# Optimization experiments

Hardware: AMD Instinct MI355X
Metric: run time of the kernel (lower is better)

Reference implementation:

```python
import jax, jax.numpy as jnp
from jax import lax
import numpy as np

B, H, W, C = 8, 32, 32, 256
SOFTMAX_SCALE = 10.0
DN = ('NHWC', 'HWIO', 'NHWC')


def _patches(t):
    # t: [b,h,w,c] -> [b,h,w,3,3,c], SAME zero padding, stride 1 (tf.image.extract_patches)
    b, h, w, c = t.shape
    tp = jnp.pad(t, ((0, 0), (1, 1), (1, 1), (0, 0)))
    cols = [tp[:, i:i + h, j:j + w, :] for i in range(3) for j in range(3)]
    return jnp.stack(cols, axis=3).reshape(b, h, w, 3, 3, c)


def _diag_fuse(z):
    # conv2d of [L,L] map with eye(3) kernel, SAME padding:
    # out[i,j] = z[i-1,j-1] + z[i,j] + z[i+1,j+1] (zero padded)
    dr = jnp.pad(z, ((1, 0), (1, 0)))[:-1, :-1]
    ul = jnp.pad(z, ((0, 1), (0, 1)))[1:, 1:]
    return z + dr + ul


def _conv(x, w):
    return lax.conv_general_dilated(x, w, (1, 1), 'SAME', dimension_numbers=DN)


def _attend(xi, wi, mmean):
    # xi: [h,w,c]; wi: [3,3,c,L] patch kernels; mmean: [L] mean of mask patches
    h, w, c = xi.shape
    L = h * w
    norm = jnp.maximum(jnp.sqrt(jnp.sum(wi * wi, axis=(0, 1, 2))), 1e-4)
    yi = _conv(xi[None], wi / norm)[0]  # [h,w,L] cosine-sim scores
    # fuse: diagonal propagation along both spatial orderings
    z = yi.reshape(L, L)
    z = _diag_fuse(z).reshape(h, w, h, w).transpose(1, 0, 3, 2).reshape(L, L)
    z = _diag_fuse(z).reshape(w, h, w, h).transpose(1, 0, 3, 2)  # [h,w,h,w]
    yi = z.reshape(h, w, L)
    mm = (mmean == 1.0).astype(yi.dtype)  # valid-patch mask per location
    yi = jax.nn.softmax(yi * mm * SOFTMAX_SCALE, axis=-1) * mm
    # conv2d_transpose(yi, wi, stride 1, SAME) == conv with hw-flipped kernel,
    # in/out channels swapped (TF filter layout [h,w,out=C,in=L])
    k2 = jnp.flip(wi, (0, 1)).transpose(0, 1, 3, 2)  # [3,3,L,C]
    return _conv(yi[None], k2)[0]  # [h,w,c]


def _forward(x, mask, conv_w, conv_b, conv1_w, conv1_b, conv2_w, conv2_b):
    b, h, w, c = x.shape
    L = h * w
    # rate=1: tf.image.resize to same size is identity, f == b == x
    wi = _patches(x).reshape(b, L, 3, 3, c).transpose(0, 2, 3, 4, 1)  # [b,3,3,c,L]
    mmean = _patches(mask).mean(axis=(3, 4, 5)).reshape(b, L)
    y = jax.vmap(_attend)(x, wi, mmean)  # [b,h,w,c]
    ycat = jnp.concatenate([y, x], axis=-1)  # [b,h,w,2c]
    g1 = jax.nn.sigmoid(_conv(ycat, conv1_w) + conv1_b)
    g2 = jax.nn.sigmoid(_conv(ycat, conv2_w) + conv2_b)
    gate = (g1 + g2) * 0.5
    out = gate * (_conv(ycat, conv_w) + conv_b)
    return out, jnp.ones_like(mask)


def setup_inputs() -> dict:
    key = jax.random.key(0)
    ks = jax.random.split(key, 4)
    x = jax.random.normal(ks[0], (B, H, W, C), jnp.float32)
    mask = jnp.ones((B, H, W, 1), jnp.float32)
    conv_w = jax.random.normal(ks[1], (3, 3, 2 * C, C), jnp.float32) * 0.02
    conv_b = jnp.zeros((C,), jnp.float32)
    conv1_w = jax.random.normal(ks[2], (1, 1, 2 * C, C), jnp.float32) * 0.02
    conv1_b = jnp.zeros((C,), jnp.float32)
    conv2_w = jax.random.normal(ks[3], (3, 3, 2 * C, C), jnp.float32) * 0.02
    conv2_b = jnp.zeros((C,), jnp.float32)
    return {'x': x, 'mask': mask, 'conv_w': conv_w, 'conv_b': conv_b,
            'conv1_w': conv1_w, 'conv1_b': conv1_b, 'conv2_w': conv2_w, 'conv2_b': conv2_b}


def reference(x, mask, conv_w, conv_b, conv1_w, conv1_b, conv2_w, conv2_b):
    return _forward(x, mask, conv_w, conv_b, conv1_w, conv1_b, conv2_w, conv2_b)
```

## Files before the change

kernel.cpp:

```cpp
#include <hip/hip_runtime.h>
#include <math.h>

typedef unsigned short u16;
typedef __bf16 bf16x8 __attribute__((ext_vector_type(8)));
typedef float f32x4 __attribute__((ext_vector_type(4)));

#define NPOS 1156
#define GSTR 1160
#define GOFF (GSTR * 1156)
#define YSTR 1032
#define YOFF (YSTR * 1026)
#define POS34(p) ((((p) >> 5) + 1) * 34 + ((p) & 31) + 1)

__device__ __constant__ const int kDiagOff[9] = {
    -35 * (GSTR + 1), -34 * (GSTR + 1), -33 * (GSTR + 1),
    -1 * (GSTR + 1),  0,                1 * (GSTR + 1),
    33 * (GSTR + 1),  34 * (GSTR + 1),  35 * (GSTR + 1)};

__device__ __forceinline__ u16 f2bf(float f) {
  unsigned int u = __builtin_bit_cast(unsigned int, f);
  return (u16)((u + 0x7FFFu + ((u >> 16) & 1u)) >> 16);
}
__device__ __forceinline__ float bf2f(u16 v) {
  unsigned int u = ((unsigned int)v) << 16;
  return __builtin_bit_cast(float, u);
}
__device__ __forceinline__ void gload16(const void* g, void* l) {
  __builtin_amdgcn_global_load_lds(
      (const __attribute__((address_space(1))) void*)g,
      (__attribute__((address_space(3))) void*)l, 16, 0, 0);
}
__device__ __forceinline__ int posOf(int p) { return POS34(p); }

__global__ __launch_bounds__(256) void cast_x(
    const float* __restrict__ x, u16* __restrict__ xpad, u16* __restrict__ xT) {
  int blk = blockIdx.x;
  int b = blk >> 5, h = blk & 31;
  __shared__ u16 T[256][33];
  const float* xrow = x + ((size_t)b * 1024 + h * 32) * 256;
  int tid = threadIdx.x;
  for (int idx = tid; idx < 8192; idx += 256) {
    int w = idx >> 8, c = idx & 255;
    u16 v = f2bf(xrow[(size_t)w * 256 + c]);
    T[c][w] = v;
    xpad[((size_t)b * NPOS + (h + 1) * 34 + (w + 1)) * 256 + c] = v;
  }
  __syncthreads();
  int c = tid;
  unsigned int* dp = (unsigned int*)(xT + ((size_t)(b * 256 + c)) * 1024 + h * 32);
  const unsigned int* sp = (const unsigned int*)&T[c][0];
#pragma unroll
  for (int u = 0; u < 16; ++u) dp[u] = sp[u];
}

__global__ __launch_bounds__(256) void wtrans(
    const float* __restrict__ src, u16* __restrict__ dst, int K) {
  int k0 = blockIdx.x * 32;
  __shared__ u16 T[256][34];
  int tid = threadIdx.x;
  for (int idx = tid; idx < 8192; idx += 256) {
    int kr = idx >> 8, c = idx & 255;
    T[c][kr] = f2bf(src[(size_t)(k0 + kr) * 256 + c]);
  }
  __syncthreads();
  int c = tid;
  unsigned int* dp = (unsigned int*)(dst + (size_t)c * K + k0);
  const unsigned int* sp = (const unsigned int*)&T[c][0];
#pragma unroll
  for (int u = 0; u < 16; ++u) dp[u] = sp[u];
}

__global__ __launch_bounds__(256) void gram_base(
    const u16* __restrict__ xpad, float* __restrict__ Gpad) {
  const int b = blockIdx.z;
  const int m0 = blockIdx.x << 7;
  const int n0 = blockIdx.y << 7;
  const u16* xb = xpad + (size_t)b * NPOS * 256;
  __shared__ __align__(16) u16 As[128 * 64];
  __shared__ __align__(16) u16 Bs[128 * 64];
  const int tid = threadIdx.x;
  const int lane = tid & 63;
  const int wave = tid >> 6;
  const int wm = wave >> 1, wn = wave & 1;
  const int srow = lane >> 3;
  const int cswz = ((lane & 7) ^ srow) << 3;
  int pa[4], pb[4];
#pragma unroll
  for (int i = 0; i < 4; ++i) {
    pa[i] = posOf(m0 + wave * 32 + i * 8 + srow);
    pb[i] = posOf(n0 + wave * 32 + i * 8 + srow);
  }
  int aidx[4][2], bidx[4][2];
#pragma unroll
  for (int f = 0; f < 4; ++f)
#pragma unroll
    for (int ks = 0; ks < 2; ++ks) {
      int ra = wm * 64 + f * 16 + (lane & 15);
      int rb = wn * 64 + f * 16 + (lane & 15);
      int k16 = ks * 4 + (lane >> 4);
      aidx[f][ks] = ra * 64 + ((k16 ^ (ra & 7)) << 3);
      bidx[f][ks] = rb * 64 + ((k16 ^ (rb & 7)) << 3);
    }
  f32x4 acc[4][4] = {};
  for (int c0 = 0; c0 < 256; c0 += 64) {
    __syncthreads();
#pragma unroll
    for (int i = 0; i < 4; ++i) {
      gload16(xb + (size_t)pa[i] * 256 + c0 + cswz, &As[(wave * 32 + i * 8) * 64]);
      gload16(xb + (size_t)pb[i] * 256 + c0 + cswz, &Bs[(wave * 32 + i * 8) * 64]);
    }
    __syncthreads();
#pragma unroll
    for (int ks = 0; ks < 2; ++ks) {
      bf16x8 a[4], bb[4];
#pragma unroll
      for (int f = 0; f < 4; ++f) a[f] = *(const bf16x8*)(As + aidx[f][ks]);
#pragma unroll
      for (int f = 0; f < 4; ++f) bb[f] = *(const bf16x8*)(Bs + bidx[f][ks]);
#pragma unroll
      for (int mi = 0; mi < 4; ++mi)
#pragma unroll
        for (int ni = 0; ni < 4; ++ni)
          acc[mi][ni] = __builtin_amdgcn_mfma_f32_16x16x32_bf16(a[mi], bb[ni], acc[mi][ni], 0, 0, 0);
    }
  }
  float* Gb = Gpad + (size_t)b * GOFF;
  const int r0 = (lane >> 4) << 2;
  const int cb0 = n0 + wn * 64 + (lane & 15);
#pragma unroll
  for (int mi = 0; mi < 4; ++mi) {
    int row = m0 + wm * 64 + mi * 16 + r0;
    int rp = POS34(row);
#pragma unroll
    for (int ni = 0; ni < 4; ++ni) {
      int cp = POS34(cb0 + ni * 16);
#pragma unroll
      for (int r = 0; r < 4; ++r)
        Gb[(size_t)(rp + r) * GSTR + cp] = acc[mi][ni][r];
    }
  }
}

__global__ __launch_bounds__(256) void norm_mm(
    const float* __restrict__ Gpad, const float* __restrict__ mask,
    float* __restrict__ invn, float* __restrict__ mm, float* __restrict__ ones_out) {
  int idx = blockIdx.x * 256 + threadIdx.x;
  int b = idx >> 10, l = idx & 1023;
  const float* Gb = Gpad + (size_t)b * GOFF;
  size_t dbase = (size_t)POS34(l) * (GSTR + 1);
  float d = 0.f;
#pragma unroll
  for (int t = 0; t < 9; ++t) d += Gb[dbase + kDiagOff[t]];
  invn[idx] = 1.0f / fmaxf(sqrtf(d), 1e-4f);
  int lh = l >> 5, lw = l & 31;
  float s = 0.f;
  for (int dh = -1; dh <= 1; ++dh)
    for (int dw = -1; dw <= 1; ++dw) {
      int hh = lh + dh, wv = lw + dw;
      if (hh >= 0 && hh < 32 && wv >= 0 && wv < 32) s += mask[b * 1024 + hh * 32 + wv];
    }
  mm[idx] = ((s / 9.0f) == 1.0f) ? 1.0f : 0.0f;
  ones_out[idx] = 1.0f;
}

__global__ __launch_bounds__(256) void patch_norm_p(
    const float* __restrict__ Gpad, const float* __restrict__ invn,
    float* __restrict__ Ylin) {
  const int b = blockIdx.y;
  const int p0 = blockIdx.x << 2;
  const float* Gb = Gpad + (size_t)b * GOFF;
  float* Yb = Ylin + (size_t)b * YOFF;
  const int tid = threadIdx.x;
  const int l0 = tid << 2;
  const int lp0 = POS34(l0);
  const float4 iv = *(const float4*)(invn + (b << 10) + l0);
#pragma unroll
  for (int r = 0; r < 4; ++r) {
    int p = p0 + r;
    int base = POS34(p) * GSTR + lp0;
    float v[9][4];
#pragma unroll
    for (int t = 0; t < 9; ++t) {
      const float* q = Gb + (base + kDiagOff[t]);
      v[t][0] = q[0]; v[t][1] = q[1]; v[t][2] = q[2]; v[t][3] = q[3];
    }
    float s0 = 0.f, s1 = 0.f, s2 = 0.f, s3 = 0.f;
#pragma unroll
    for (int t = 0; t < 9; ++t) { s0 += v[t][0]; s1 += v[t][1]; s2 += v[t][2]; s3 += v[t][3]; }
    float* yw = Yb + (size_t)(p + 1) * YSTR + l0 + 1;
    yw[0] = s0 * iv.x; yw[1] = s1 * iv.y; yw[2] = s2 * iv.z; yw[3] = s3 * iv.w;
  }
}

__device__ __forceinline__ float z1p(const float* __restrict__ Yb, int r, int c) {
  size_t a = (size_t)(r + 1) * YSTR + (c + 1);
  return Yb[a] + Yb[a - (YSTR + 1)] + Yb[a + (YSTR + 1)];
}

__global__ __launch_bounds__(256) void fuse_softmax(
    const float* __restrict__ Ylin, const float* __restrict__ mm,
    float* __restrict__ Apad2) {
  const int bi = blockIdx.x;
  const int b = bi >> 10, i = bi & 1023;
  const float* Yb = Ylin + (size_t)b * YOFF;
  __shared__ float smm[1024];
  __shared__ float red[256];
  const int tid = threadIdx.x;
  for (int t = tid; t < 1024; t += 256) smm[t] = mm[(b << 10) + t];
  __syncthreads();
  const int si = ((i & 31) << 5) | (i >> 5);
  const int rm = (si >= 1) ? ((((si - 1) & 31) << 5) | ((si - 1) >> 5)) : -1;
  const int rp = (si <= 1022) ? ((((si + 1) & 31) << 5) | ((si + 1) >> 5)) : -1;
  float logit[4];
  float lmax = -3.0e38f;
#pragma unroll
  for (int q = 0; q < 4; ++q) {
    int j = tid + (q << 8);
    int sj = ((j & 31) << 5) | (j >> 5);
    float S = z1p(Yb, i, j);
    if (rm >= 0 && sj >= 1) {
      int col = (((sj - 1) & 31) << 5) | ((sj - 1) >> 5);
      S += z1p(Yb, rm, col);
    }
    if (rp >= 0 && sj <= 1022) {
      int col = (((sj + 1) & 31) << 5) | ((sj + 1) >> 5);
      S += z1p(Yb, rp, col);
    }
    float lg = S * smm[j] * 10.0f;
    logit[q] = lg;
    lmax = fmaxf(lmax, lg);
  }
  red[tid] = lmax; __syncthreads();
  for (int off = 128; off > 0; off >>= 1) {
    if (tid < off) red[tid] = fmaxf(red[tid], red[tid + off]);
    __syncthreads();
  }
  float M = red[0];
  __syncthreads();
  float ex[4];
  float lsum = 0.f;
#pragma unroll
  for (int q = 0; q < 4; ++q) { ex[q] = expf(logit[q] - M); lsum += ex[q]; }
  red[tid] = lsum; __syncthreads();
  for (int off = 128; off > 0; off >>= 1) {
    if (tid < off) red[tid] += red[tid + off];
    __syncthreads();
  }
  float inv = 1.0f / red[0];
  float* Ap = Apad2 + (size_t)b * GOFF + (size_t)POS34(i) * GSTR;
#pragma unroll
  for (int q = 0; q < 4; ++q) {
    int j = tid + (q << 8);
    Ap[POS34(j)] = smm[j] * ex[q] * inv;
  }
}

__global__ __launch_bounds__(256) void afuse_p(
    const float* __restrict__ Apad2, u16* __restrict__ Afuse) {
  const int b = blockIdx.y;
  const int q0 = blockIdx.x << 2;
  const float* Ab = Apad2 + (size_t)b * GOFF;
  u16* Fb = Afuse + ((size_t)b << 20);
  const int tid = threadIdx.x;
  const int l0 = tid << 2;
  const int lp0 = POS34(l0);
#pragma unroll
  for (int r = 0; r < 4; ++r) {
    int q = q0 + r;
    int base = POS34(q) * GSTR + lp0;
    float v[9][4];
#pragma unroll
    for (int t = 0; t < 9; ++t) {
      const float* p = Ab + (base - kDiagOff[t]);
      v[t][0] = p[0]; v[t][1] = p[1]; v[t][2] = p[2]; v[t][3] = p[3];
    }
    float s0 = 0.f, s1 = 0.f, s2 = 0.f, s3 = 0.f;
#pragma unroll
    for (int t = 0; t < 9; ++t) { s0 += v[t][0]; s1 += v[t][1]; s2 += v[t][2]; s3 += v[t][3]; }
    u16* fw = Fb + (size_t)q * 1024 + l0;
    fw[0] = f2bf(s0); fw[1] = f2bf(s1); fw[2] = f2bf(s2); fw[3] = f2bf(s3);
  }
}

__global__ __launch_bounds__(256) void paste_gemm(
    const u16* __restrict__ Afuse, const u16* __restrict__ xT, u16* __restrict__ ypad) {
  const int bm0 = blockIdx.x << 6;
  const int b = bm0 >> 10;
  const int q0 = bm0 & 1023;
  const int n0 = blockIdx.y << 6;
  const u16* Ab = Afuse + ((size_t)b << 20);
  const u16* xTb = xT + ((size_t)b << 18);
  __shared__ __align__(16) u16 As[64 * 64];
  __shared__ __align__(16) u16 Bs[64 * 64];
  const int tid = threadIdx.x;
  const int lane = tid & 63;
  const int wave = tid >> 6;
  const int wm = wave >> 1, wn = wave & 1;
  const int srow = lane >> 3;
  const int cswz = ((lane & 7) ^ srow) << 3;
  int aidx[2][2], bidx[2][2];
#pragma unroll
  for (int ks = 0; ks < 2; ++ks) {
    int k16 = ks * 4 + (lane >> 4);
#pragma unroll
    for (int f = 0; f < 2; ++f) {
      int ra = wm * 32 + f * 16 + (lane & 15);
      aidx[f][ks] = ra * 64 + ((k16 ^ (ra & 7)) << 3);
      int rb = wn * 32 + f * 16 + (lane & 15);
      bidx[f][ks] = rb * 64 + ((k16 ^ (rb & 7)) << 3);
    }
  }
  f32x4 acc[2][2] = {};
  for (int l0 = 0; l0 < 1024; l0 += 64) {
    __syncthreads();
#pragma unroll
    for (int i = 0; i < 2; ++i) {
      int ar = wave * 16 + i * 8 + srow;
      gload16(Ab + (size_t)(q0 + ar) * 1024 + l0 + cswz, &As[ar * 64]);
      gload16(xTb + (size_t)(n0 + ar) * 1024 + l0 + cswz, &Bs[ar * 64]);
    }
    __syncthreads();
#pragma unroll
    for (int ks = 0; ks < 2; ++ks) {
      bf16x8 a[2], bb[2];
#pragma unroll
      for (int f = 0; f < 2; ++f) a[f] = *(const bf16x8*)(As + aidx[f][ks]);
#pragma unroll
      for (int f = 0; f < 2; ++f) bb[f] = *(const bf16x8*)(Bs + bidx[f][ks]);
#pragma unroll
      for (int mi = 0; mi < 2; ++mi)
#pragma unroll
        for (int ni = 0; ni < 2; ++ni)
          acc[mi][ni] = __builtin_amdgcn_mfma_f32_16x16x32_bf16(a[mi], bb[ni], acc[mi][ni], 0, 0, 0);
    }
  }
  u16* yb = ypad + (size_t)b * NPOS * 256;
  const int r0 = (lane >> 4) << 2;
#pragma unroll
  for (int mi = 0; mi < 2; ++mi) {
    int qb = q0 + wm * 32 + mi * 16 + r0;
#pragma unroll
    for (int ni = 0; ni < 2; ++ni) {
      int c = n0 + wn * 32 + ni * 16 + (lane & 15);
#pragma unroll
      for (int r = 0; r < 4; ++r)
        yb[(size_t)posOf(qb + r) * 256 + c] = f2bf(acc[mi][ni][r]);
    }
  }
}

__global__ __launch_bounds__(256) void final_fused(
    const u16* __restrict__ ypad, const u16* __restrict__ xpad,
    const u16* __restrict__ w0T, const u16* __restrict__ w1T,
    const u16* __restrict__ w2T,
    const float* __restrict__ b0, const float* __restrict__ b1,
    const float* __restrict__ b2, float* __restrict__ out) {
  const int m0 = blockIdx.x << 6;
  const int b = m0 >> 10;
  const int q0 = m0 & 1023;
  const int n0 = blockIdx.y << 6;
  const u16* yb = ypad + (size_t)b * NPOS * 256;
  const u16* xb = xpad + (size_t)b * NPOS * 256;
  __shared__ __align__(16) u16 As[64 * 64];
  __shared__ __align__(16) u16 B0s[64 * 64];
  __shared__ __align__(16) u16 B1s[64 * 64];
  __shared__ __align__(16) u16 B2s[64 * 64];
  const int tid = threadIdx.x;
  const int lane = tid & 63;
  const int wave = tid >> 6;
  const int wm = wave >> 1, wn = wave & 1;
  const int srow = lane >> 3;
  const int cswz = ((lane & 7) ^ srow) << 3;
  int posA[2];
#pragma unroll
  for (int i = 0; i < 2; ++i) posA[i] = posOf(q0 + wave * 16 + i * 8 + srow);
  int aidx[2][2], bidx[2][2];
#pragma unroll
  for (int ks = 0; ks < 2; ++ks) {
    int k16 = ks * 4 + (lane >> 4);
#pragma unroll
    for (int f = 0; f < 2; ++f) {
      int ra = wm * 32 + f * 16 + (lane & 15);
      aidx[f][ks] = ra * 64 + ((k16 ^ (ra & 7)) << 3);
      int rb = wn * 32 + f * 16 + (lane & 15);
      bidx[f][ks] = rb * 64 + ((k16 ^ (rb & 7)) << 3);
    }
  }
  f32x4 acc0[2][2] = {}, acc1[2][2] = {}, acc2[2][2] = {};
  for (int s = 0; s < 9; ++s) {
    const int dpos = (s / 3 - 1) * 34 + (s % 3 - 1);
    for (int c0 = 0; c0 < 512; c0 += 64) {
      const u16* base = (c0 < 256) ? yb : xb;
      const int coff = c0 & 255;
      __syncthreads();
#pragma unroll
      for (int i = 0; i < 2; ++i) {
        int ar = wave * 16 + i * 8 + srow;
        gload16(base + (size_t)(posA[i] + dpos) * 256 + coff + cswz, &As[ar * 64]);
        size_t krow = (size_t)(n0 + ar) * 4608 + s * 512 + c0 + cswz;
        gload16(w0T + krow, &B0s[ar * 64]);
        gload16(w2T + krow, &B2s[ar * 64]);
        if (s == 4)
          gload16(w1T + (size_t)(n0 + ar) * 512 + c0 + cswz, &B1s[ar * 64]);
      }
      __syncthreads();
#pragma unroll
      for (int ks = 0; ks < 2; ++ks) {
        bf16x8 a[2], v0[2], v2[2];
#pragma unroll
        for (int f = 0; f < 2; ++f) a[f] = *(const bf16x8*)(As + aidx[f][ks]);
#pragma unroll
        for (int f = 0; f < 2; ++f) v0[f] = *(const bf16x8*)(B0s + bidx[f][ks]);
#pragma unroll
        for (int f = 0; f < 2; ++f) v2[f] = *(const bf16x8*)(B2s + bidx[f][ks]);
#pragma unroll
        for (int mi = 0; mi < 2; ++mi)
#pragma unroll
          for (int ni = 0; ni < 2; ++ni) {
            acc0[mi][ni] = __builtin_amdgcn_mfma_f32_16x16x32_bf16(a[mi], v0[ni], acc0[mi][ni], 0, 0, 0);
            acc2[mi][ni] = __builtin_amdgcn_mfma_f32_16x16x32_bf16(a[mi], v2[ni], acc2[mi][ni], 0, 0, 0);
          }
        if (s == 4) {
          bf16x8 v1[2];
#pragma unroll
          for (int f = 0; f < 2; ++f) v1[f] = *(const bf16x8*)(B1s + bidx[f][ks]);
#pragma unroll
          for (int mi = 0; mi < 2; ++mi)
#pragma unroll
            for (int ni = 0; ni < 2; ++ni)
              acc1[mi][ni] = __builtin_amdgcn_mfma_f32_16x16x32_bf16(a[mi], v1[ni], acc1[mi][ni], 0, 0, 0);
        }
      }
    }
  }
  const int r0 = (lane >> 4) << 2;
#pragma unroll
  for (int ni = 0; ni < 2; ++ni) {
    int co = n0 + wn * 32 + ni * 16 + (lane & 15);
    float q0b = b0[co], q1b = b1[co], q2b = b2[co];
#pragma unroll
    for (int mi = 0; mi < 2; ++mi) {
      int m = m0 + wm * 32 + mi * 16 + r0;
#pragma unroll
      for (int r = 0; r < 4; ++r) {
        float g1 = 1.f / (1.f + expf(-(acc1[mi][ni][r] + q1b)));
        float g2 = 1.f / (1.f + expf(-(acc2[mi][ni][r] + q2b)));
        out[(size_t)(m + r) * 256 + co] = 0.5f * (g1 + g2) * (acc0[mi][ni][r] + q0b);
      }
    }
  }
}


extern "C" void kernel_launch(void* const* d_in, const int* in_sizes, int n_in,
                              void* d_out, int out_size, void* d_ws, size_t ws_size,
                              hipStream_t stream) {
  const float* x = (const float*)d_in[0];
  const float* mask = (const float*)d_in[1];
  const float* conv_w = (const float*)d_in[2];
  const float* conv_b = (const float*)d_in[3];
  const float* conv1_w = (const float*)d_in[4];
  const float* conv1_b = (const float*)d_in[5];
  const float* conv2_w = (const float*)d_in[6];
  const float* conv2_b = (const float*)d_in[7];
  float* out = (float*)d_out;
  char* wsb = (char*)d_ws;

  float* Gpad  = (float*)(wsb + 0);
  float* Apad2 = (float*)(wsb + 0);
  float* Ylin  = (float*)(wsb + 42910720);
  u16* Afuse   = (u16*)(wsb + 42910720);
  u16* xpad    = (u16*)(wsb + 76793344);
  u16* ypad    = (u16*)(wsb + 81528320);
  u16* xT      = (u16*)(wsb + 86263296);
  u16* w0T     = (u16*)(wsb + 90457600);
  u16* w2T     = (u16*)(wsb + 92816896);
  u16* w1T     = (u16*)(wsb + 95176192);
  float* invn  = (float*)(wsb + 95438336);
  float* mmb   = (float*)(wsb + 95471104);

  hipMemsetAsync(wsb, 0, 76793344, stream);
  hipMemsetAsync(wsb + 76793344, 0, 9469952, stream);

  cast_x<<<256, 256, 0, stream>>>(x, xpad, xT);
  wtrans<<<144, 256, 0, stream>>>(conv_w, w0T, 4608);
  wtrans<<<144, 256, 0, stream>>>(conv2_w, w2T, 4608);
  wtrans<<<16, 256, 0, stream>>>(conv1_w, w1T, 512);

  gram_base<<<dim3(8, 8, 8), 256, 0, stream>>>(xpad, Gpad);
  norm_mm<<<32, 256, 0, stream>>>(Gpad, mask, invn, mmb, out + 2097152);
  patch_norm_p<<<dim3(256, 8), 256, 0, stream>>>(Gpad, invn, Ylin);
  fuse_softmax<<<8192, 256, 0, stream>>>(Ylin, mmb, Apad2);
  afuse_p<<<dim3(256, 8), 256, 0, stream>>>(Apad2, Afuse);
  paste_gemm<<<dim3(128, 4), 256, 0, stream>>>(Afuse, xT, ypad);
  final_fused<<<dim3(128, 4), 256, 0, stream>>>(ypad, xpad, w0T, w1T, w2T,
                                                conv_b, conv1_b, conv2_b, out);
}
```

Measured before the change: 281.7 us.

## Store score and attention intermediates in bf16 and double-buffer GEMM LDS tiles

Changes the Ylin score map and the Apad2 attention buffer from fp32 to bf16. This roughly halves the memory traffic of patch_norm_p, fuse_softmax and afuse_p, and shrinks the workspace memset, at the cost of precision in the softmax inputs. It also adds a second memset to re-zero the Apad2 padding region before fuse_softmax, because that region now aliases the Gpad buffer. Separately, paste_gemm and final_fused get double-buffered shared-memory tiles so the next tile loads while MFMAs run on the current one, which doubles their LDS footprint.

```diff
diff --git a/kernel.cpp b/kernel.cpp
--- a/kernel.cpp
+++ b/kernel.cpp
@@ -165,11 +165,11 @@
 
 __global__ __launch_bounds__(256) void patch_norm_p(
     const float* __restrict__ Gpad, const float* __restrict__ invn,
-    float* __restrict__ Ylin) {
+    u16* __restrict__ Ylin) {
   const int b = blockIdx.y;
   const int p0 = blockIdx.x << 2;
   const float* Gb = Gpad + (size_t)b * GOFF;
-  float* Yb = Ylin + (size_t)b * YOFF;
+  u16* Yb = Ylin + (size_t)b * YOFF;
   const int tid = threadIdx.x;
   const int l0 = tid << 2;
   const int lp0 = POS34(l0);
@@ -187,22 +187,23 @@
     float s0 = 0.f, s1 = 0.f, s2 = 0.f, s3 = 0.f;
 #pragma unroll
     for (int t = 0; t < 9; ++t) { s0 += v[t][0]; s1 += v[t][1]; s2 += v[t][2]; s3 += v[t][3]; }
-    float* yw = Yb + (size_t)(p + 1) * YSTR + l0 + 1;
-    yw[0] = s0 * iv.x; yw[1] = s1 * iv.y; yw[2] = s2 * iv.z; yw[3] = s3 * iv.w;
-  }
-}
-
-__device__ __forceinline__ float z1p(const float* __restrict__ Yb, int r, int c) {
+    u16* yw = Yb + (size_t)(p + 1) * YSTR + l0 + 1;
+    yw[0] = f2bf(s0 * iv.x); yw[1] = f2bf(s1 * iv.y);
+    yw[2] = f2bf(s2 * iv.z); yw[3] = f2bf(s3 * iv.w);
+  }
+}
+
+__device__ __forceinline__ float z1p(const u16* __restrict__ Yb, int r, int c) {
   size_t a = (size_t)(r + 1) * YSTR + (c + 1);
-  return Yb[a] + Yb[a - (YSTR + 1)] + Yb[a + (YSTR + 1)];
+  return bf2f(Yb[a]) + bf2f(Yb[a - (YSTR + 1)]) + bf2f(Yb[a + (YSTR + 1)]);
 }
 
 __global__ __launch_bounds__(256) void fuse_softmax(
-    const float* __restrict__ Ylin, const float* __restrict__ mm,
-    float* __restrict__ Apad2) {
+    const u16* __restrict__ Ylin, const float* __restrict__ mm,
+    u16* __restrict__ Apad2) {
   const int bi = blockIdx.x;
   const int b = bi >> 10, i = bi & 1023;
-  const float* Yb = Ylin + (size_t)b * YOFF;
+  const u16* Yb = Ylin + (size_t)b * YOFF;
   __shared__ float smm[1024];
   __shared__ float red[256];
   const int tid = threadIdx.x;
@@ -247,19 +248,19 @@
     __syncthreads();
   }
   float inv = 1.0f / red[0];
-  float* Ap = Apad2 + (size_t)b * GOFF + (size_t)POS34(i) * GSTR;
+  u16* Ap = Apad2 + (size_t)b * GOFF + (size_t)POS34(i) * GSTR;
 #pragma unroll
   for (int q = 0; q < 4; ++q) {
     int j = tid + (q << 8);
-    Ap[POS34(j)] = smm[j] * ex[q] * inv;
+    Ap[POS34(j)] = f2bf(smm[j] * ex[q] * inv);
   }
 }
 
 __global__ __launch_bounds__(256) void afuse_p(
-    const float* __restrict__ Apad2, u16* __restrict__ Afuse) {
+    const u16* __restrict__ Apad2, u16* __restrict__ Afuse) {
   const int b = blockIdx.y;
   const int q0 = blockIdx.x << 2;
-  const float* Ab = Apad2 + (size_t)b * GOFF;
+  const u16* Ab = Apad2 + (size_t)b * GOFF;
   u16* Fb = Afuse + ((size_t)b << 20);
   const int tid = threadIdx.x;
   const int l0 = tid << 2;
@@ -271,8 +272,9 @@
     float v[9][4];
 #pragma unroll
     for (int t = 0; t < 9; ++t) {
-      const float* p = Ab + (base - kDiagOff[t]);
-      v[t][0] = p[0]; v[t][1] = p[1]; v[t][2] = p[2]; v[t][3] = p[3];
+      const u16* p = Ab + (base - kDiagOff[t]);
+      v[t][0] = bf2f(p[0]); v[t][1] = bf2f(p[1]);
+      v[t][2] = bf2f(p[2]); v[t][3] = bf2f(p[3]);
     }
     float s0 = 0.f, s1 = 0.f, s2 = 0.f, s3 = 0.f;
 #pragma unroll
@@ -290,8 +292,8 @@
   const int n0 = blockIdx.y << 6;
   const u16* Ab = Afuse + ((size_t)b << 20);
   const u16* xTb = xT + ((size_t)b << 18);
-  __shared__ __align__(16) u16 As[64 * 64];
-  __shared__ __align__(16) u16 Bs[64 * 64];
+  __shared__ __align__(16) u16 As[2][64 * 64];
+  __shared__ __align__(16) u16 Bs[2][64 * 64];
   const int tid = threadIdx.x;
   const int lane = tid & 63;
   const int wave = tid >> 6;
@@ -310,29 +312,35 @@
       bidx[f][ks] = rb * 64 + ((k16 ^ (rb & 7)) << 3);
     }
   }
-  f32x4 acc[2][2] = {};
-  for (int l0 = 0; l0 < 1024; l0 += 64) {
-    __syncthreads();
+  auto STAGE = [&](int kt, int pb) {
+    int l0 = kt << 6;
 #pragma unroll
     for (int i = 0; i < 2; ++i) {
       int ar = wave * 16 + i * 8 + srow;
-      gload16(Ab + (size_t)(q0 + ar) * 1024 + l0 + cswz, &As[ar * 64]);
-      gload16(xTb + (size_t)(n0 + ar) * 1024 + l0 + cswz, &Bs[ar * 64]);
-    }
-    __syncthreads();
+      gload16(Ab + (size_t)(q0 + ar) * 1024 + l0 + cswz, &As[pb][ar * 64]);
+      gload16(xTb + (size_t)(n0 + ar) * 1024 + l0 + cswz, &Bs[pb][ar * 64]);
+    }
+  };
+  f32x4 acc[2][2] = {};
+  STAGE(0, 0);
+  __syncthreads();
+  for (int kt = 0; kt < 16; ++kt) {
+    int pb = kt & 1;
+    if (kt < 15) STAGE(kt + 1, pb ^ 1);
 #pragma unroll
     for (int ks = 0; ks < 2; ++ks) {
       bf16x8 a[2], bb[2];
 #pragma unroll
-      for (int f = 0; f < 2; ++f) a[f] = *(const bf16x8*)(As + aidx[f][ks]);
-#pragma unroll
-      for (int f = 0; f < 2; ++f) bb[f] = *(const bf16x8*)(Bs + bidx[f][ks]);
+      for (int f = 0; f < 2; ++f) a[f] = *(const bf16x8*)(&As[pb][0] + aidx[f][ks]);
+#pragma unroll
+      for (int f = 0; f < 2; ++f) bb[f] = *(const bf16x8*)(&Bs[pb][0] + bidx[f][ks]);
 #pragma unroll
       for (int mi = 0; mi < 2; ++mi)
 #pragma unroll
         for (int ni = 0; ni < 2; ++ni)
           acc[mi][ni] = __builtin_amdgcn_mfma_f32_16x16x32_bf16(a[mi], bb[ni], acc[mi][ni], 0, 0, 0);
     }
+    __syncthreads();
   }
   u16* yb = ypad + (size_t)b * NPOS * 256;
   const int r0 = (lane >> 4) << 2;
@@ -361,10 +369,10 @@
   const int n0 = blockIdx.y << 6;
   const u16* yb = ypad + (size_t)b * NPOS * 256;
   const u16* xb = xpad + (size_t)b * NPOS * 256;
-  __shared__ __align__(16) u16 As[64 * 64];
-  __shared__ __align__(16) u16 B0s[64 * 64];
-  __shared__ __align__(16) u16 B1s[64 * 64];
-  __shared__ __align__(16) u16 B2s[64 * 64];
+  __shared__ __align__(16) u16 As[2][64 * 64];
+  __shared__ __align__(16) u16 B0s[2][64 * 64];
+  __shared__ __align__(16) u16 B1s[2][64 * 64];
+  __shared__ __align__(16) u16 B2s[2][64 * 64];
   const int tid = threadIdx.x;
   const int lane = tid & 63;
   const int wave = tid >> 6;
@@ -386,52 +394,58 @@
       bidx[f][ks] = rb * 64 + ((k16 ^ (rb & 7)) << 3);
     }
   }
+  auto STAGE = [&](int kt, int pb) {
+    int s = kt >> 3;
+    int c0k = (kt & 7) << 6;
+    const u16* basep = (c0k < 256) ? yb : xb;
+    int coff = c0k & 255;
+    int dpos = (s / 3 - 1) * 34 + (s % 3 - 1);
+#pragma unroll
+    for (int i = 0; i < 2; ++i) {
+      int ar = wave * 16 + i * 8 + srow;
+      gload16(basep + (size_t)(posA[i] + dpos) * 256 + coff + cswz, &As[pb][ar * 64]);
+      size_t krow = (size_t)(n0 + ar) * 4608 + s * 512 + c0k + cswz;
+      gload16(w0T + krow, &B0s[pb][ar * 64]);
+      gload16(w2T + krow, &B2s[pb][ar * 64]);
+      if (s == 4)
+        gload16(w1T + (size_t)(n0 + ar) * 512 + c0k + cswz, &B1s[pb][ar * 64]);
+    }
+  };
   f32x4 acc0[2][2] = {}, acc1[2][2] = {}, acc2[2][2] = {};
-  for (int s = 0; s < 9; ++s) {
-    const int dpos = (s / 3 - 1) * 34 + (s % 3 - 1);
-    for (int c0 = 0; c0 < 512; c0 += 64) {
-      const u16* base = (c0 < 256) ? yb : xb;
-      const int coff = c0 & 255;
-      __syncthreads();
-#pragma unroll
-      for (int i = 0; i < 2; ++i) {
-        int ar = wave * 16 + i * 8 + srow;
-        gload16(base + (size_t)(posA[i] + dpos) * 256 + coff + cswz, &As[ar * 64]);
-        size_t krow = (size_t)(n0 + ar) * 4608 + s * 512 + c0 + cswz;
-        gload16(w0T + krow, &B0s[ar * 64]);
-        gload16(w2T + krow, &B2s[ar * 64]);
-        if (s == 4)
-          gload16(w1T + (size_t)(n0 + ar) * 512 + c0 + cswz, &B1s[ar * 64]);
+  STAGE(0, 0);
+  __syncthreads();
+  for (int kt = 0; kt < 72; ++kt) {
+    const int pb = kt & 1;
+    if (kt < 71) STAGE(kt + 1, pb ^ 1);
+    const int s = kt >> 3;
+#pragma unroll
+    for (int ks = 0; ks < 2; ++ks) {
+      bf16x8 a[2], v0[2], v2[2];
+#pragma unroll
+      for (int f = 0; f < 2; ++f) a[f] = *(const bf16x8*)(&As[pb][0] + aidx[f][ks]);
+#pragma unroll
+      for (int f = 0; f < 2; ++f) v0[f] = *(const bf16x8*)(&B0s[pb][0] + bidx[f][ks]);
+#pragma unroll
+      for (int f = 0; f < 2; ++f) v2[f] = *(const bf16x8*)(&B2s[pb][0] + bidx[f][ks]);
+#pragma unroll
+      for (int mi = 0; mi < 2; ++mi)
+#pragma unroll
+        for (int ni = 0; ni < 2; ++ni) {
+          acc0[mi][ni] = __builtin_amdgcn_mfma_f32_16x16x32_bf16(a[mi], v0[ni], acc0[mi][ni], 0, 0, 0);
+          acc2[mi][ni] = __builtin_amdgcn_mfma_f32_16x16x32_bf16(a[mi], v2[ni], acc2[mi][ni], 0, 0, 0);
+        }
+      if (s == 4) {
+        bf16x8 v1[2];
+#pragma unroll
+        for (int f = 0; f < 2; ++f) v1[f] = *(const bf16x8*)(&B1s[pb][0] + bidx[f][ks]);
+#pragma unroll
+        for (int mi = 0; mi < 2; ++mi)
+#pragma unroll
+          for (int ni = 0; ni < 2; ++ni)
+            acc1[mi][ni] = __builtin_amdgcn_mfma_f32_16x16x32_bf16(a[mi], v1[ni], acc1[mi][ni], 0, 0, 0);
       }
-      __syncthreads();
-#pragma unroll
-      for (int ks = 0; ks < 2; ++ks) {
-        bf16x8 a[2], v0[2], v2[2];
-#pragma unroll
-        for (int f = 0; f < 2; ++f) a[f] = *(const bf16x8*)(As + aidx[f][ks]);
-#pragma unroll
-        for (int f = 0; f < 2; ++f) v0[f] = *(const bf16x8*)(B0s + bidx[f][ks]);
-#pragma unroll
-        for (int f = 0; f < 2; ++f) v2[f] = *(const bf16x8*)(B2s + bidx[f][ks]);
-#pragma unroll
-        for (int mi = 0; mi < 2; ++mi)
-#pragma unroll
-          for (int ni = 0; ni < 2; ++ni) {
-            acc0[mi][ni] = __builtin_amdgcn_mfma_f32_16x16x32_bf16(a[mi], v0[ni], acc0[mi][ni], 0, 0, 0);
-            acc2[mi][ni] = __builtin_amdgcn_mfma_f32_16x16x32_bf16(a[mi], v2[ni], acc2[mi][ni], 0, 0, 0);
-          }
-        if (s == 4) {
-          bf16x8 v1[2];
-#pragma unroll
-          for (int f = 0; f < 2; ++f) v1[f] = *(const bf16x8*)(B1s + bidx[f][ks]);
-#pragma unroll
-          for (int mi = 0; mi < 2; ++mi)
-#pragma unroll
-            for (int ni = 0; ni < 2; ++ni)
-              acc1[mi][ni] = __builtin_amdgcn_mfma_f32_16x16x32_bf16(a[mi], v1[ni], acc1[mi][ni], 0, 0, 0);
-        }
-      }
-    }
+    }
+    __syncthreads();
   }
   const int r0 = (lane >> 4) << 2;
 #pragma unroll
@@ -467,20 +481,19 @@
   char* wsb = (char*)d_ws;
 
   float* Gpad  = (float*)(wsb + 0);
-  float* Apad2 = (float*)(wsb + 0);
-  float* Ylin  = (float*)(wsb + 42910720);
+  u16* Apad2   = (u16*)(wsb + 0);
+  u16* Ylin    = (u16*)(wsb + 42910720);
   u16* Afuse   = (u16*)(wsb + 42910720);
-  u16* xpad    = (u16*)(wsb + 76793344);
-  u16* ypad    = (u16*)(wsb + 81528320);
-  u16* xT      = (u16*)(wsb + 86263296);
-  u16* w0T     = (u16*)(wsb + 90457600);
-  u16* w2T     = (u16*)(wsb + 92816896);
-  u16* w1T     = (u16*)(wsb + 95176192);
-  float* invn  = (float*)(wsb + 95438336);
-  float* mmb   = (float*)(wsb + 95471104);
-
-  hipMemsetAsync(wsb, 0, 76793344, stream);
-  hipMemsetAsync(wsb + 76793344, 0, 9469952, stream);
+  u16* xpad    = (u16*)(wsb + 59852032);
+  u16* ypad    = (u16*)(wsb + 64587008);
+  u16* xT      = (u16*)(wsb + 69321984);
+  u16* w0T     = (u16*)(wsb + 73516288);
+  u16* w2T     = (u16*)(wsb + 75875584);
+  u16* w1T     = (u16*)(wsb + 78234880);
+  float* invn  = (float*)(wsb + 78497024);
+  float* mmb   = (float*)(wsb + 78529792);
+
+  hipMemsetAsync(wsb, 0, 69321984, stream);
 
   cast_x<<<256, 256, 0, stream>>>(x, xpad, xT);
   wtrans<<<144, 256, 0, stream>>>(conv_w, w0T, 4608);
@@ -490,6 +503,7 @@
   gram_base<<<dim3(8, 8, 8), 256, 0, stream>>>(xpad, Gpad);
   norm_mm<<<32, 256, 0, stream>>>(Gpad, mask, invn, mmb, out + 2097152);
   patch_norm_p<<<dim3(256, 8), 256, 0, stream>>>(Gpad, invn, Ylin);
+  hipMemsetAsync(wsb, 0, 21455360, stream);
   fuse_softmax<<<8192, 256, 0, stream>>>(Ylin, mmb, Apad2);
   afuse_p<<<dim3(256, 8), 256, 0, stream>>>(Apad2, Afuse);
   paste_gemm<<<dim3(128, 4), 256, 0, stream>>>(Afuse, xT, ypad);
```

After: 281.8 us. No clear change (+0.0%).
